# Kernel tuning notes

Measured on AMD Instinct MI355X. Metric: run time of the kernel, lower is better.

## Reference

```python
import jax, jax.numpy as jnp
import numpy as np

# LIF constants (LIFParams defaults, normalized units)
V_REST = 0.0
V_TH = 1.0
R = 1.0
DT = 1.0
TAU = 10.0
SLOPE = 5.0  # surrogate heaviside slope

N_INPUT, N_HIDDEN, N_OUTPUT = 784, 256, 10
BATCH, T = 128, 500


def setup_inputs() -> dict:
    key = jax.random.key(0)
    k1, k2, k3 = jax.random.split(key, 3)
    input_spikes = jax.random.uniform(k1, (BATCH, N_INPUT, T), dtype=jnp.float32)
    w_input_hidden = jax.random.uniform(k2, (N_INPUT, N_HIDDEN), dtype=jnp.float32) * 0.1
    w_hidden_output = jax.random.uniform(k3, (N_HIDDEN, N_OUTPUT), dtype=jnp.float32) * 0.1
    return {"input_spikes": input_spikes,
            "w_input_hidden": w_input_hidden,
            "w_hidden_output": w_hidden_output}


def reference(input_spikes, w_input_hidden, w_hidden_output):
    # input_spikes: (B, n_input, T)
    batch = input_spikes.shape[0]
    # relu(weight) computed once (original recomputes per step)
    w_ih = jax.nn.relu(w_input_hidden)
    w_ho = jax.nn.relu(w_hidden_output)
    alpha_h = DT / TAU
    alpha_o = DT / TAU

    xs = jnp.transpose(input_spikes, (2, 0, 1))  # (T, B, n_input)

    def step(carry, x_t):
        v_h, v_o = carry
        I_h = x_t @ w_ih                              # (B, n_hidden)
        v_h = v_h + (-(v_h - V_REST) + R * I_h) * alpha_h
        s_h = jax.nn.sigmoid(SLOPE * (v_h - V_TH))
        I_o = s_h @ w_ho                              # (B, n_output)
        v_o = v_o + (-(v_o - V_REST) + R * I_o) * alpha_o
        s_o = jax.nn.sigmoid(SLOPE * (v_o - V_TH))
        return (v_h, v_o), s_o

    v_h0 = jnp.full((batch, N_HIDDEN), V_REST, dtype=input_spikes.dtype)
    v_o0 = jnp.full((batch, N_OUTPUT), V_REST, dtype=input_spikes.dtype)
    _, out_seq = jax.lax.scan(step, (v_h0, v_o0), xs)   # (T, B, n_output)
    output_spikes = jnp.transpose(out_seq, (1, 2, 0))    # (B, n_output, T)
    firing_rates = output_spikes.mean(axis=2)            # (B, n_output)
    return output_spikes, firing_rates
```

## Files before the change

kernel.cpp:

```cpp
#include <hip/hip_runtime.h>


typedef __attribute__((ext_vector_type(4))) float  floatx4;
typedef __attribute__((ext_vector_type(8))) short  shortx8;
typedef unsigned short u16;
typedef unsigned int   u32;

#define B_   128
#define NIN  784
#define NH   256
#define NO   10
#define T_   500
#define NK   25

__device__ __forceinline__ u16 f2bf(float f) {
    union { float f; u32 u; } x; x.f = f;
    u32 r = x.u + 0x7FFFu + ((x.u >> 16) & 1u);
    return (u16)(r >> 16);
}
__device__ __forceinline__ float bf2f(u16 u) {
    union { u32 u; float f; } x; x.u = ((u32)u) << 16; return x.f;
}
__device__ __forceinline__ float sigmoid5(float v) {
    return 1.0f / (1.0f + __expf(-5.0f * (v - 1.0f)));
}

__device__ __forceinline__ void gload16(const u16* g, u16* l) {
    __builtin_amdgcn_global_load_lds(
        (const __attribute__((address_space(1))) unsigned int*)(const void*)g,
        (__attribute__((address_space(3))) unsigned int*)(void*)l, 16, 0, 0);
}

__global__ void convert_W(const float* __restrict__ w_ih,
                          const float* __restrict__ w_ho,
                          u16* __restrict__ Bt, float* __restrict__ wrelu) {
    if (blockIdx.x == NK * 32) {
        for (int i = threadIdx.x; i < NH * NO; i += 256)
            wrelu[i] = fmaxf(0.f, w_ho[i]);
        return;
    }
    const int k = blockIdx.x;
    const int n = threadIdx.x;
    const float f = (k < NIN) ? fmaxf(0.f, w_ih[k * NH + n]) : 0.f;
    const int kt = k >> 5, kk = k & 31;
    const int slot = (kk >> 3) ^ (n & 3) ^ ((n >> 2) & 3);
    Bt[(size_t)kt * 8192 + n * 32 + slot * 8 + (kk & 7)] = f2bf(f);
}

__global__ __launch_bounds__(1024, 4) void gemm_hidden(
    const float* __restrict__ spikes,
    const u16* __restrict__ Bt,
    u16* __restrict__ Ih)
{
    __shared__ u16 SH[32768];
    u16* AS0 = SH;
    u16* AS1 = SH + 8192;
    u16* BS0 = SH + 16384;
    u16* BS1 = SH + 24576;

    const int tid = threadIdx.x;
    const int b   = blockIdx.x >> 1;
    const int th  = blockIdx.x & 1;
    const int t0  = th * 256;

    const int kq = tid >> 6, tg = tid & 63;
    const int tloc = t0 + tg * 4;
    const bool t_ok = (tloc <= 496);
    const float* sbase = spikes + (size_t)b * (NIN * T_) + tloc;
    const int oct  = kq >> 2;
    const int koff = (2 * kq) & 7;

    const int lane = tid & 63, wid = tid >> 6;
    const int wm = wid >> 2, wn = wid & 3;
    const int lg = lane >> 4, lr = lane & 15;
    int aOff[4], bOff[4];
#pragma unroll
    for (int mi = 0; mi < 4; ++mi) {
        const int m = wm * 64 + mi * 16 + lr;
        aOff[mi] = m * 32 + ((lg ^ (m & 3) ^ ((m >> 2) & 3)) << 3);
    }
#pragma unroll
    for (int ni = 0; ni < 4; ++ni) {
        const int n = wn * 64 + ni * 16 + lr;
        bOff[ni] = n * 32 + ((lg ^ (n & 3) ^ ((n >> 2) & 3)) << 3);
    }

    floatx4 acc[4][4];
#pragma unroll
    for (int i = 0; i < 4; ++i)
#pragma unroll
        for (int j = 0; j < 4; ++j) acc[i][j] = (floatx4)0.f;

#define LOADA(v0, v1, itv) {                                                   \
        const int gk = (itv) * 32 + 2 * kq;                                    \
        const bool ok0 = t_ok && (gk < NIN);                                   \
        const bool ok1 = t_ok && (gk + 1 < NIN);                               \
        const float* p0 = ok0 ? (sbase + (size_t)gk * T_) : sbase;             \
        const float* p1 = ok1 ? (sbase + (size_t)(gk + 1) * T_) : sbase;       \
        floatx4 u0 = *(const floatx4*)p0;                                      \
        floatx4 u1 = *(const floatx4*)p1;                                      \
        v0 = ok0 ? u0 : (floatx4)0.f;                                          \
        v1 = ok1 ? u1 : (floatx4)0.f; }

#define WRITEA(ASX, v0, v1) { _Pragma("unroll") for (int j = 0; j < 4; ++j) {  \
        const int m = tg * 4 + j;                                              \
        const int slot = oct ^ (m & 3) ^ ((m >> 2) & 3);                       \
        const u32 pk = (u32)f2bf(v0[j]) | ((u32)f2bf(v1[j]) << 16);            \
        *(u32*)&(ASX)[m * 32 + slot * 8 + koff] = pk; } }

#define STAGEB(BSX, itv)                                                       \
        gload16(Bt + (size_t)(itv) * 8192 + tid * 8, (BSX) + tid * 8);

#define MFMAIT(ASX, BSX) { shortx8 af[4], bf[4];                               \
        _Pragma("unroll") for (int mi = 0; mi < 4; ++mi)                       \
            af[mi] = *(const shortx8*)&(ASX)[aOff[mi]];                        \
        _Pragma("unroll") for (int ni = 0; ni < 4; ++ni)                       \
            bf[ni] = *(const shortx8*)&(BSX)[bOff[ni]];                        \
        _Pragma("unroll") for (int mi = 0; mi < 4; ++mi)                       \
        _Pragma("unroll") for (int ni = 0; ni < 4; ++ni)                       \
            acc[mi][ni] = __builtin_amdgcn_mfma_f32_16x16x32_bf16(             \
                af[mi], bf[ni], acc[mi][ni], 0, 0, 0); }

#define CBAR2 { asm volatile("s_waitcnt vmcnt(2) lgkmcnt(0)" ::: "memory");    \
                __builtin_amdgcn_s_barrier(); }
#define LBAR  { asm volatile("s_waitcnt lgkmcnt(0)" ::: "memory");             \
                __builtin_amdgcn_s_barrier(); }

    floatx4 vaP0, vaP1;

    LOADA(vaP0, vaP1, 0);
    WRITEA(AS0, vaP0, vaP1);
    STAGEB(BS0, 0);
    LOADA(vaP0, vaP1, 1);
    CBAR2;

    for (int it = 0; it < 24; it += 2) {
        STAGEB(BS1, it + 1);
        WRITEA(AS1, vaP0, vaP1);
        { const int nv = (it + 2 < 24) ? (it + 2) : 24;
          LOADA(vaP0, vaP1, nv); }
        MFMAIT(AS0, BS0);
        CBAR2;

        STAGEB(BS0, it + 2);
        WRITEA(AS0, vaP0, vaP1);
        { const int nv = (it + 3 < 24) ? (it + 3) : 24;
          LOADA(vaP0, vaP1, nv); }
        MFMAIT(AS1, BS1);
        CBAR2;
    }
    MFMAIT(AS0, BS0);
    LBAR;

    u16* Cs = SH;
#pragma unroll
    for (int h = 0; h < 4; ++h) {
        if (wm == h) {
#pragma unroll
            for (int mi = 0; mi < 4; ++mi)
#pragma unroll
                for (int rr = 0; rr < 2; ++rr) {
                    const int mloc = mi * 16 + lg * 4 + rr * 2;
#pragma unroll
                    for (int ni = 0; ni < 4; ++ni) {
                        const int n = wn * 64 + ni * 16 + lr;
                        const u32 pk = (u32)f2bf(acc[mi][ni][rr * 2]) |
                                       ((u32)f2bf(acc[mi][ni][rr * 2 + 1]) << 16);
                        *(u32*)&Cs[n * 64 + (mloc ^ ((n & 7) << 3))] = pk;
                    }
                }
        }
        LBAR;
        {
            const int n = tid >> 2, ms = tid & 3;
            u16* gdst = Ih + ((size_t)b * 256 + n) * 512 + t0 + h * 64 + ms * 16;
#pragma unroll
            for (int j = 0; j < 2; ++j) {
                const uint4 v = *(const uint4*)&Cs[n * 64 +
                                ((ms * 16 + j * 8) ^ ((n & 7) << 3))];
                *(uint4*)(gdst + j * 8) = v;
            }
        }
        LBAR;
    }
#undef LOADA
#undef WRITEA
#undef STAGEB
#undef MFMAIT
#undef CBAR2
#undef LBAR
}

__global__ __launch_bounds__(512) void scan_h(u16* __restrict__ Ih) {
    const int lane = threadIdx.x & 63;
    const int row  = blockIdx.x * 8 + (threadIdx.x >> 6);
    u16* p = Ih + (size_t)row * 512 + lane * 8;
    shortx8 xv = *(const shortx8*)p;
    float I[8];
#pragma unroll
    for (int j = 0; j < 8; ++j) I[j] = bf2f((u16)xv[j]);
    float z = 0.f;
#pragma unroll
    for (int j = 0; j < 8; ++j) z += (I[j] - z) * 0.1f;
    float A = 0.43046721f, Bv = z;
#pragma unroll
    for (int d = 1; d < 64; d <<= 1) {
        const float Au = __shfl_up(A, d);
        const float Bu = __shfl_up(Bv, d);
        if (lane >= d) { Bv = fmaf(A, Bu, Bv); A *= Au; }
    }
    float v = __shfl_up(Bv, 1);
    if (lane == 0) v = 0.f;
#pragma unroll
    for (int j = 0; j < 8; ++j) {
        v += (I[j] - v) * 0.1f;
        xv[j] = (short)f2bf(sigmoid5(v));
    }
    *(shortx8*)p = xv;
}

__global__ __launch_bounds__(512) void gemm_out(
    const u16* __restrict__ s,
    const float* __restrict__ wr,
    float* __restrict__ Io)
{
    __shared__ float P[4][128][NO];
    const int tid = threadIdx.x;
    const int b   = blockIdx.x >> 2;
    const int tq  = blockIdx.x & 3;
    const int hq  = tid >> 7;
    const int tl  = tid & 127;
    const int t   = tq * 128 + tl;

    float acc[NO];
#pragma unroll
    for (int o = 0; o < NO; ++o) acc[o] = 0.f;
    const u16* sb = s + ((size_t)b * NH + hq * 64) * 512 + t;
    const float* wb = wr + hq * 64 * NO;
#pragma unroll 4
    for (int h = 0; h < 64; ++h) {
        const float sv = bf2f(sb[h * 512]);
#pragma unroll
        for (int o = 0; o < NO; ++o) acc[o] = fmaf(sv, wb[h * NO + o], acc[o]);
    }
#pragma unroll
    for (int o = 0; o < NO; ++o) P[hq][tl][o] = acc[o];
    __syncthreads();

    for (int i = tid; i < 128 * NO; i += 512) {
        const int tt = i / NO, o = i - tt * NO;
        const int tg = tq * 128 + tt;
        if (tg < T_)
            Io[((size_t)b * T_ + tg) * NO + o] =
                P[0][tt][o] + P[1][tt][o] + P[2][tt][o] + P[3][tt][o];
    }
}

__global__ __launch_bounds__(256) void lif_out(
    const float* __restrict__ IoG,
    float* __restrict__ out)
{
    __shared__ float Io[T_ * NO];
    __shared__ float vend[25][NO], vstart[25][NO], psum[25][NO];
    const int b = blockIdx.x, tid = threadIdx.x;

    for (int i = tid; i < T_ * NO; i += 256)
        Io[i] = IoG[(size_t)b * (T_ * NO) + i];
    __syncthreads();

    const int seg = tid / NO, o = tid - seg * NO;
    if (tid < 250) {
        float v = 0.f;
#pragma unroll
        for (int j = 0; j < 20; ++j)
            v += (Io[(seg * 20 + j) * NO + o] - v) * 0.1f;
        vend[seg][o] = v;
    }
    __syncthreads();
    if (tid < NO) {
        float vs = 0.f;
#pragma unroll
        for (int sg = 0; sg < 25; ++sg) {
            vstart[sg][tid] = vs;
            vs = vend[sg][tid] + 0.12157665459f * vs;
        }
    }
    __syncthreads();
    if (tid < 250) {
        float v = vstart[seg][o], ps = 0.f;
#pragma unroll
        for (int j = 0; j < 20; ++j) {
            const int t = seg * 20 + j;
            v += (Io[t * NO + o] - v) * 0.1f;
            const float sv = sigmoid5(v);
            out[(size_t)b * (NO * T_) + (size_t)o * T_ + t] = sv;
            ps += sv;
        }
        psum[seg][o] = ps;
    }
    __syncthreads();
    if (tid < NO) {
        float tot = 0.f;
#pragma unroll
        for (int sg = 0; sg < 25; ++sg) tot += psum[sg][tid];
        out[(size_t)(B_ * NO) * T_ + b * NO + tid] = tot * (1.0f / T_);
    }
}

extern "C" void kernel_launch(void* const* d_in, const int* in_sizes, int n_in,
                              void* d_out, int out_size, void* d_ws, size_t ws_size,
                              hipStream_t stream) {
    (void)in_sizes; (void)n_in; (void)out_size; (void)ws_size;
    const float* spikes = (const float*)d_in[0];
    const float* w_ih   = (const float*)d_in[1];
    const float* w_ho   = (const float*)d_in[2];
    float* out = (float*)d_out;

    float* wrelu = (float*)d_ws;
    u16*   Bt    = (u16*)((char*)d_ws + 16384);
    u16*   Ih    = (u16*)((char*)d_ws + 524288);
    float* Io    = (float*)((char*)d_ws + 524288 + 33554432);

    convert_W  <<<NK * 32 + 1, 256, 0, stream>>>(w_ih, w_ho, Bt, wrelu);
    gemm_hidden<<<256, 1024, 0, stream>>>(spikes, Bt, Ih);
    scan_h     <<<4096, 512, 0, stream>>>(Ih);
    gemm_out   <<<512, 512, 0, stream>>>(Ih, wrelu, Io);
    lif_out    <<<B_, 256, 0, stream>>>(Io, out);
}
```

Measured before the change: 95.49 us.

## Fuse hidden scan with output GEMM via LDS and MFMA, remap blocks to XCDs

Result: faster. 82.01 us, median of 2 (-14.1%).

```diff
diff --git a/kernel.cpp b/kernel.cpp
--- a/kernel.cpp
+++ b/kernel.cpp
@@ -12,6 +12,7 @@
 #define NO   10
 #define T_   500
 #define NK   25
+#define SROW 520
 
 __device__ __forceinline__ u16 f2bf(float f) {
     union { float f; u32 u; } x; x.f = f;
@@ -59,9 +60,11 @@
     u16* BS1 = SH + 24576;
 
     const int tid = threadIdx.x;
-    const int b   = blockIdx.x >> 1;
-    const int th  = blockIdx.x & 1;
-    const int t0  = th * 256;
+    const int xcd  = blockIdx.x & 7;
+    const int slot = blockIdx.x >> 3;
+    const int b    = xcd * 16 + (slot >> 1);
+    const int th   = slot & 1;
+    const int t0   = th * 256;
 
     const int kq = tid >> 6, tg = tid & 63;
     const int tloc = t0 + tg * 4;
@@ -104,9 +107,9 @@
 
 #define WRITEA(ASX, v0, v1) { _Pragma("unroll") for (int j = 0; j < 4; ++j) {  \
         const int m = tg * 4 + j;                                              \
-        const int slot = oct ^ (m & 3) ^ ((m >> 2) & 3);                       \
+        const int slt = oct ^ (m & 3) ^ ((m >> 2) & 3);                        \
         const u32 pk = (u32)f2bf(v0[j]) | ((u32)f2bf(v1[j]) << 16);            \
-        *(u32*)&(ASX)[m * 32 + slot * 8 + koff] = pk; } }
+        *(u32*)&(ASX)[m * 32 + slt * 8 + koff] = pk; } }
 
 #define STAGEB(BSX, itv)                                                       \
         gload16(Bt + (size_t)(itv) * 8192 + tid * 8, (BSX) + tid * 8);
@@ -191,81 +194,96 @@
 #undef LBAR
 }
 
-__global__ __launch_bounds__(512) void scan_h(u16* __restrict__ Ih) {
-    const int lane = threadIdx.x & 63;
-    const int row  = blockIdx.x * 8 + (threadIdx.x >> 6);
-    u16* p = Ih + (size_t)row * 512 + lane * 8;
-    shortx8 xv = *(const shortx8*)p;
-    float I[8];
-#pragma unroll
-    for (int j = 0; j < 8; ++j) I[j] = bf2f((u16)xv[j]);
-    float z = 0.f;
-#pragma unroll
-    for (int j = 0; j < 8; ++j) z += (I[j] - z) * 0.1f;
-    float A = 0.43046721f, Bv = z;
-#pragma unroll
-    for (int d = 1; d < 64; d <<= 1) {
-        const float Au = __shfl_up(A, d);
-        const float Bu = __shfl_up(Bv, d);
-        if (lane >= d) { Bv = fmaf(A, Bu, Bv); A *= Au; }
-    }
-    float v = __shfl_up(Bv, 1);
-    if (lane == 0) v = 0.f;
+__global__ __launch_bounds__(512, 2) void scan_dot(
+    const u16* __restrict__ Ih,
+    const float* __restrict__ wr,
+    float* __restrict__ IoP)
+{
+    __shared__ u16 sbuf[64 * SROW];
+    const int tid = threadIdx.x;
+    const int hg  = blockIdx.x & 3;
+    const int b   = blockIdx.x >> 2;
+    const int h0  = hg * 64;
+    const int lane = tid & 63, w = tid >> 6;
+
+    for (int r = 0; r < 8; ++r) {
+        const int hl = w * 8 + r;
+        const u16* p = Ih + ((size_t)b * 256 + h0 + hl) * 512 + lane * 8;
+        shortx8 xv = *(const shortx8*)p;
+        float I[8];
+#pragma unroll
+        for (int j = 0; j < 8; ++j) I[j] = bf2f((u16)xv[j]);
+        float z = 0.f;
+#pragma unroll
+        for (int j = 0; j < 8; ++j) z += (I[j] - z) * 0.1f;
+        float A = 0.43046721f, Bv = z;
+#pragma unroll
+        for (int d = 1; d < 64; d <<= 1) {
+            const float Au = __shfl_up(A, d);
+            const float Bu = __shfl_up(Bv, d);
+            if (lane >= d) { Bv = fmaf(A, Bu, Bv); A *= Au; }
+        }
+        float v = __shfl_up(Bv, 1);
+        if (lane == 0) v = 0.f;
+        shortx8 sv;
+#pragma unroll
+        for (int j = 0; j < 8; ++j) {
+            v += (I[j] - v) * 0.1f;
+            sv[j] = (short)f2bf(sigmoid5(v));
+        }
+        *(shortx8*)&sbuf[hl * SROW + lane * 8] = sv;
+    }
+    __syncthreads();
+
+    const int lg = lane >> 4, lr = lane & 15;
+    shortx8 bw0, bw1;
 #pragma unroll
     for (int j = 0; j < 8; ++j) {
-        v += (I[j] - v) * 0.1f;
-        xv[j] = (short)f2bf(sigmoid5(v));
-    }
-    *(shortx8*)p = xv;
-}
-
-__global__ __launch_bounds__(512) void gemm_out(
-    const u16* __restrict__ s,
-    const float* __restrict__ wr,
-    float* __restrict__ Io)
-{
-    __shared__ float P[4][128][NO];
-    const int tid = threadIdx.x;
-    const int b   = blockIdx.x >> 2;
-    const int tq  = blockIdx.x & 3;
-    const int hq  = tid >> 7;
-    const int tl  = tid & 127;
-    const int t   = tq * 128 + tl;
-
-    float acc[NO];
-#pragma unroll
-    for (int o = 0; o < NO; ++o) acc[o] = 0.f;
-    const u16* sb = s + ((size_t)b * NH + hq * 64) * 512 + t;
-    const float* wb = wr + hq * 64 * NO;
-#pragma unroll 4
-    for (int h = 0; h < 64; ++h) {
-        const float sv = bf2f(sb[h * 512]);
-#pragma unroll
-        for (int o = 0; o < NO; ++o) acc[o] = fmaf(sv, wb[h * NO + o], acc[o]);
-    }
-#pragma unroll
-    for (int o = 0; o < NO; ++o) P[hq][tl][o] = acc[o];
-    __syncthreads();
-
-    for (int i = tid; i < 128 * NO; i += 512) {
-        const int tt = i / NO, o = i - tt * NO;
-        const int tg = tq * 128 + tt;
-        if (tg < T_)
-            Io[((size_t)b * T_ + tg) * NO + o] =
-                P[0][tt][o] + P[1][tt][o] + P[2][tt][o] + P[3][tt][o];
+        const int hA = h0 + lg * 8 + j;
+        const int hB = hA + 32;
+        bw0[j] = (short)((lr < NO) ? f2bf(wr[hA * NO + lr]) : 0);
+        bw1[j] = (short)((lr < NO) ? f2bf(wr[hB * NO + lr]) : 0);
+    }
+#pragma unroll
+    for (int fi = 0; fi < 4; ++fi) {
+        const int tf = w * 4 + fi;
+        const int t  = tf * 16 + lr;
+        floatx4 acc = (floatx4)0.f;
+#pragma unroll
+        for (int ks = 0; ks < 2; ++ks) {
+            union { shortx8 s; u32 d[4]; } u;
+#pragma unroll
+            for (int q = 0; q < 4; ++q) {
+                const int h1 = ks * 32 + lg * 8 + 2 * q;
+                u.d[q] = (u32)sbuf[h1 * SROW + t] |
+                         ((u32)sbuf[(h1 + 1) * SROW + t] << 16);
+            }
+            acc = __builtin_amdgcn_mfma_f32_16x16x32_bf16(
+                u.s, (ks == 0) ? bw0 : bw1, acc, 0, 0, 0);
+        }
+        if (lr < NO) {
+#pragma unroll
+            for (int rr = 0; rr < 4; ++rr) {
+                const int tt = tf * 16 + lg * 4 + rr;
+                IoP[(((size_t)b * 512 + tt) * 4 + hg) * NO + lr] = acc[rr];
+            }
+        }
     }
 }
 
 __global__ __launch_bounds__(256) void lif_out(
-    const float* __restrict__ IoG,
+    const float* __restrict__ IoP,
     float* __restrict__ out)
 {
     __shared__ float Io[T_ * NO];
     __shared__ float vend[25][NO], vstart[25][NO], psum[25][NO];
     const int b = blockIdx.x, tid = threadIdx.x;
 
-    for (int i = tid; i < T_ * NO; i += 256)
-        Io[i] = IoG[(size_t)b * (T_ * NO) + i];
+    for (int i = tid; i < T_ * NO; i += 256) {
+        const int t = i / NO, o = i - t * NO;
+        const float* q = IoP + ((size_t)b * 512 + t) * 40 + o;
+        Io[i] = (q[0] + q[10]) + (q[20] + q[30]);
+    }
     __syncthreads();
 
     const int seg = tid / NO, o = tid - seg * NO;
@@ -319,11 +337,10 @@
     float* wrelu = (float*)d_ws;
     u16*   Bt    = (u16*)((char*)d_ws + 16384);
     u16*   Ih    = (u16*)((char*)d_ws + 524288);
-    float* Io    = (float*)((char*)d_ws + 524288 + 33554432);
+    float* IoP   = (float*)((char*)d_ws + 524288 + 33554432);
 
     convert_W  <<<NK * 32 + 1, 256, 0, stream>>>(w_ih, w_ho, Bt, wrelu);
     gemm_hidden<<<256, 1024, 0, stream>>>(spikes, Bt, Ih);
-    scan_h     <<<4096, 512, 0, stream>>>(Ih);
-    gemm_out   <<<512, 512, 0, stream>>>(Ih, wrelu, Io);
-    lif_out    <<<B_, 256, 0, stream>>>(Io, out);
-}
+    scan_dot   <<<512, 512, 0, stream>>>(Ih, wrelu, IoP);
+    lif_out    <<<B_, 256, 0, stream>>>(IoP, out);
+}
```
